# Performance work log

Hardware: AMD Instinct MI355X
Metric: run time of the kernel (lower is better)

The kernel has to match this reference:

```python
import jax, jax.numpy as jnp
import numpy as np

TEMP = 0.5   # temperature from __init__
EPS = 1e-8   # torch.nn.CosineSimilarity eps


def setup_inputs() -> dict:
    key = jax.random.key(0)
    N, D = 8192, 256
    x = jax.random.normal(key, (N, D), dtype=jnp.float32)
    # pairs: each label appears exactly twice, as required for the
    # sim[~mask].reshape(N, -1) in the original to be well-formed
    y = jnp.arange(N, dtype=jnp.int32) // 2
    return {"x": x, "y": y}


def reference(x, y):
    # cosine similarity matrix: normalize once, then one NxD @ DxN matmul
    # (equivalent to CosineSimilarity(x.unsqueeze(1), x.unsqueeze(0)) without
    #  the NxNxD intermediate)
    norm = jnp.maximum(jnp.linalg.norm(x, axis=1, keepdims=True), EPS)
    xn = x / norm
    sim = (xn @ xn.T) / TEMP                     # [N, N]

    # Original: positives = equal-label entries (row-major order, includes the
    # diagonal), logits = [positives | negatives] which is just a per-row
    # permutation of sim; labels = 0 -> CE target is the FIRST equal-label
    # column of each row. logsumexp is over the full row (all N entries).
    eq = y[:, None] == y[None, :]                # [N, N] bool
    first_pos = jnp.argmax(eq, axis=1)           # first column j with y_j == y_i
    target = jnp.take_along_axis(sim, first_pos[:, None], axis=1)[:, 0]  # [N]

    lse = jax.nn.logsumexp(sim, axis=1)          # [N]
    N = x.shape[0]
    loss = jnp.sum(lse - target) / N             # CrossEntropyLoss(sum) / N
    return loss
```

## Files before the change

### kernel.cpp

```cpp
#include <hip/hip_runtime.h>
#include <hip/hip_bf16.h>

#define D 256
#define INV_TEMP 2.0f

typedef __attribute__((ext_vector_type(8))) short short8;
typedef __attribute__((ext_vector_type(4))) float floatx4;
typedef __attribute__((ext_vector_type(4))) unsigned short ushortx4;

__device__ __forceinline__ unsigned short f2bf(float f) {
    union { float f; unsigned u; } a; a.f = f;
    unsigned r = (a.u + 0x7fffu + ((a.u >> 16) & 1u)) >> 16;
    return (unsigned short)r;
}

__device__ __forceinline__ void gload_lds16(const unsigned short* g,
                                            unsigned short* l) {
    __builtin_amdgcn_global_load_lds(
        (const __attribute__((address_space(1))) unsigned int*)g,
        (__attribute__((address_space(3))) unsigned int*)l, 16, 0, 0);
}

__global__ void nt_prep_kernel(const float* __restrict__ x,
                               unsigned short* __restrict__ xnb,
                               float* __restrict__ pair_dot,
                               float* __restrict__ rowsum,
                               float* __restrict__ gsum,
                               unsigned int* __restrict__ gcnt) {
    if (blockIdx.x == 0 && threadIdx.x == 0) { *gsum = 0.f; *gcnt = 0u; }
    if (blockIdx.x < 32) rowsum[blockIdx.x * 256 + threadIdx.x] = 0.f;
    int p    = blockIdx.x * 4 + (threadIdx.x >> 6);
    int lane = threadIdx.x & 63;
    const float4* a4 = (const float4*)(x + (size_t)(2 * p) * D);
    const float4* b4 = (const float4*)(x + (size_t)(2 * p + 1) * D);
    float4 a = a4[lane], b = b4[lane];
    float saa = a.x * a.x + a.y * a.y + a.z * a.z + a.w * a.w;
    float sbb = b.x * b.x + b.y * b.y + b.z * b.z + b.w * b.w;
    float sab = a.x * b.x + a.y * b.y + a.z * b.z + a.w * b.w;
    #pragma unroll
    for (int off = 32; off; off >>= 1) {
        saa += __shfl_xor(saa, off);
        sbb += __shfl_xor(sbb, off);
        sab += __shfl_xor(sab, off);
    }
    float inva = 1.0f / fmaxf(sqrtf(saa), 1e-8f);
    float invb = 1.0f / fmaxf(sqrtf(sbb), 1e-8f);
    ushortx4 oa, ob;
    oa.x = f2bf(a.x * inva); oa.y = f2bf(a.y * inva);
    oa.z = f2bf(a.z * inva); oa.w = f2bf(a.w * inva);
    ob.x = f2bf(b.x * invb); ob.y = f2bf(b.y * invb);
    ob.z = f2bf(b.z * invb); ob.w = f2bf(b.w * invb);
    __builtin_nontemporal_store(oa, (ushortx4*)(xnb + (size_t)(2 * p) * D) + lane);
    __builtin_nontemporal_store(ob, (ushortx4*)(xnb + (size_t)(2 * p + 1) * D) + lane);
    if (lane == 0)
        pair_dot[p] = sab * inva * invb * INV_TEMP;
}

__global__ __launch_bounds__(256, 2)
void nt_simexp_kernel(const unsigned short* __restrict__ xnb,
                      float* __restrict__ rowsum) {
    __shared__ __align__(16) unsigned short Bs[128 * 256];
    __shared__ __align__(16) unsigned short As[2][128 * 32];

    const int p  = blockIdx.x >> 4, q = blockIdx.x & 15;
    const int s1 = 63 - p;
    const int c0 = 64 - p;
    const int q0 = (p + q) & 15;

    const int tid  = threadIdx.x;
    const int wave = tid >> 6, lane = tid & 63;
    const int wm   = wave & 1, wn = wave >> 1;
    const int quad = lane >> 4, c = lane & 15;

    auto strip_of = [&](int i) { return (i < c0) ? p : s1; };
    auto bi_of    = [&](int i) { return (i < c0) ? (p + i) : (s1 + i - c0); };

    auto load_B = [&](int bj) {
        const unsigned short* src = xnb + (size_t)(bj * 128) * D;
        int rs = lane >> 5, pp = lane & 31;
        #pragma unroll
        for (int t = 0; t < 16; ++t) {
            int wl = wave * 16 + t;
            int rr = wl * 2 + rs;
            int j  = (pp & ~7) | ((pp ^ rr) & 7);
            gload_lds16(src + (size_t)rr * D + j * 8, Bs + wl * 512 + lane * 8);
        }
    };
    auto load_A = [&](int bi, int ph, unsigned short* Ab) {
        const unsigned short* src = xnb + (size_t)(bi * 128) * D + ph * 32;
        int rl = lane >> 2, pq = lane & 3;
        #pragma unroll
        for (int t = 0; t < 2; ++t) {
            int wl = wave * 2 + t;
            int rr = wl * 16 + rl;
            int j  = pq ^ ((rr >> 1) & 3);
            gload_lds16(src + (size_t)rr * D + j * 8, Ab + wl * 512 + lane * 8);
        }
    };

    floatx4 acc[4][4];
    auto compute = [&](const unsigned short* Ab, int ph) {
        const int pA = quad ^ ((c >> 1) & 3);
        const int jg = ph * 4 + quad;
        const int pB = (jg & ~7) | ((jg ^ c) & 7);
        short8 af[4], bf[4];
        #pragma unroll
        for (int mt = 0; mt < 4; ++mt)
            af[mt] = *(const short8*)(Ab + (wm * 64 + mt * 16 + c) * 32 + pA * 8);
        #pragma unroll
        for (int nt = 0; nt < 4; ++nt)
            bf[nt] = *(const short8*)(Bs + (wn * 64 + nt * 16 + c) * 256 + pB * 8);
        #pragma unroll
        for (int mt = 0; mt < 4; ++mt)
            #pragma unroll
            for (int nt = 0; nt < 4; ++nt)
                acc[mt][nt] = __builtin_amdgcn_mfma_f32_16x16x32_bf16(
                    af[mt], bf[nt], acc[mt][nt], 0, 0, 0);
    };

    int bj = strip_of(q0);
    load_B(bj);
    load_A(bi_of(q0), 0, As[0]);
    __syncthreads();

    for (int i = q0; i < 65; i += 16) {
        const int bi = bi_of(i);
        const int ni = i + 16;
        const bool have_next = (ni < 65);
        const int nbj = have_next ? strip_of(ni) : -1;
        const bool same = have_next && (nbj == bj);

        #pragma unroll
        for (int mt = 0; mt < 4; ++mt)
            #pragma unroll
            for (int nt = 0; nt < 4; ++nt)
                acc[mt][nt] = (floatx4){0.f, 0.f, 0.f, 0.f};

        #pragma unroll
        for (int ph = 0; ph < 8; ++ph) {
            if (ph < 7) load_A(bi, ph + 1, As[(ph + 1) & 1]);
            else if (same) load_A(bi_of(ni), 0, As[0]);
            compute(As[ph & 1], ph);
            __syncthreads();
        }

        if (have_next && !same) {
            load_B(nbj);
            load_A(bi_of(ni), 0, As[0]);
        }

        #pragma unroll
        for (int mt = 0; mt < 4; ++mt)
            #pragma unroll
            for (int nt = 0; nt < 4; ++nt)
                #pragma unroll
                for (int r = 0; r < 4; ++r)
                    acc[mt][nt][r] = __expf(acc[mt][nt][r] * INV_TEMP);

        #pragma unroll
        for (int mt = 0; mt < 4; ++mt) {
            float ps[4] = {0.f, 0.f, 0.f, 0.f};
            #pragma unroll
            for (int nt = 0; nt < 4; ++nt)
                #pragma unroll
                for (int r = 0; r < 4; ++r)
                    ps[r] += acc[mt][nt][r];
            #pragma unroll
            for (int off = 1; off < 16; off <<= 1)
                #pragma unroll
                for (int r = 0; r < 4; ++r)
                    ps[r] += __shfl_xor(ps[r], off);
            if (c < 4) {
                float v = (c == 0) ? ps[0] : (c == 1) ? ps[1]
                        : (c == 2) ? ps[2] : ps[3];
                atomicAdd(&rowsum[bi * 128 + wm * 64 + mt * 16 + quad * 4 + c], v);
            }
        }
        if (bi != bj) {
            #pragma unroll
            for (int nt = 0; nt < 4; ++nt) {
                float cs = 0.f;
                #pragma unroll
                for (int mt = 0; mt < 4; ++mt)
                    #pragma unroll
                    for (int r = 0; r < 4; ++r)
                        cs += acc[mt][nt][r];
                cs += __shfl_xor(cs, 16);
                cs += __shfl_xor(cs, 32);
                if (quad == 0)
                    atomicAdd(&rowsum[bj * 128 + wn * 64 + nt * 16 + c], cs);
            }
        }
        if (have_next && !same) {
            __syncthreads();
            bj = nbj;
        }
    }
}

__global__ void nt_reduce_kernel(const float* __restrict__ rowsum,
                                 const float* __restrict__ pair_dot,
                                 float* __restrict__ gsum,
                                 unsigned int* __restrict__ gcnt,
                                 float* __restrict__ out, int N) {
    __shared__ float sm[8];
    int r = blockIdx.x * 512 + threadIdx.x;
    float v = logf(rowsum[r]);
    if (r & 1) v -= pair_dot[r >> 1];
    #pragma unroll
    for (int off = 32; off; off >>= 1) v += __shfl_xor(v, off);
    int lane = threadIdx.x & 63, wv = threadIdx.x >> 6;
    if (lane == 0) sm[wv] = v;
    __syncthreads();
    if (threadIdx.x == 0) {
        float s = sm[0] + sm[1] + sm[2] + sm[3]
                + sm[4] + sm[5] + sm[6] + sm[7];
        atomicAdd(gsum, s);
        __threadfence();
        if (atomicAdd(gcnt, 1u) == 15u) {
            __threadfence();
            float t = atomicAdd(gsum, 0.0f);
            out[0] = (t - (float)N) / (float)N;
        }
    }
}

extern "C" void kernel_launch(void* const* d_in, const int* in_sizes, int n_in,
                              void* d_out, int out_size, void* d_ws, size_t ws_size,
                              hipStream_t stream) {
    const float* x = (const float*)d_in[0];
    int N = in_sizes[0] / D;

    char* ws = (char*)d_ws;
    unsigned short* xnb = (unsigned short*)ws;
    float* pair_dot  = (float*)(ws + (size_t)N * D * 2);
    float* rowsum    = pair_dot + N / 2;
    float* gsum      = rowsum + N;
    unsigned int* gcnt = (unsigned int*)(gsum + 1);

    nt_prep_kernel<<<N / 8, 256, 0, stream>>>(x, xnb, pair_dot, rowsum,
                                              gsum, gcnt);
    nt_simexp_kernel<<<512, 256, 0, stream>>>(xnb, rowsum);
    nt_reduce_kernel<<<16, 512, 0, stream>>>(rowsum, pair_dot, gsum, gcnt,
                                             (float*)d_out, N);
}
```

Measured before the change: 101.8 us.

## Use 256x256 lower-triangular tiles with 4-stage K pipeline in sim-exp kernel

Replaces the persistent strip-based 128x128 tile schedule with one block per 256x256 lower-triangular tile (528 blocks of 512 threads), mapped from the block index through a triangular-number inverse with an XCD-style remap. A and B K-slices are streamed through a 4-deep LDS ring buffer using vmcnt waits and raw barriers, and s_setprio is raised around the MFMA section. The larger tiles are meant to cut global/LDS traffic per FLOP and to remove the per-tile B reload and sync overhead. In exchange the diagonal-tile waste is larger, register pressure grows with 8x4 accumulators per wave, and the explicit vmcnt counting must match the number of outstanding loads.

```diff
diff --git a/kernel.cpp b/kernel.cpp
--- a/kernel.cpp
+++ b/kernel.cpp
@@ -56,144 +56,126 @@
         pair_dot[p] = sab * inva * invb * INV_TEMP;
 }
 
-__global__ __launch_bounds__(256, 2)
+__global__ __launch_bounds__(512, 2)
 void nt_simexp_kernel(const unsigned short* __restrict__ xnb,
                       float* __restrict__ rowsum) {
-    __shared__ __align__(16) unsigned short Bs[128 * 256];
-    __shared__ __align__(16) unsigned short As[2][128 * 32];
-
-    const int p  = blockIdx.x >> 4, q = blockIdx.x & 15;
-    const int s1 = 63 - p;
-    const int c0 = 64 - p;
-    const int q0 = (p + q) & 15;
+    __shared__ __align__(16) unsigned short As[4][256 * 32];
+    __shared__ __align__(16) unsigned short Bs[4][256 * 32];
+
+    int b = (int)blockIdx.x;
+    b = (b & 7) * 66 + (b >> 3);
+    int ti = (int)((sqrtf(8.f * (float)b + 1.f) - 1.f) * 0.5f);
+    while ((ti + 1) * (ti + 2) / 2 <= b) ++ti;
+    while (ti * (ti + 1) / 2 > b) --ti;
+    const int tj = b - ti * (ti + 1) / 2;
 
     const int tid  = threadIdx.x;
     const int wave = tid >> 6, lane = tid & 63;
-    const int wm   = wave & 1, wn = wave >> 1;
+    const int wm   = wave >> 2, wn = wave & 3;
     const int quad = lane >> 4, c = lane & 15;
-
-    auto strip_of = [&](int i) { return (i < c0) ? p : s1; };
-    auto bi_of    = [&](int i) { return (i < c0) ? (p + i) : (s1 + i - c0); };
-
-    auto load_B = [&](int bj) {
-        const unsigned short* src = xnb + (size_t)(bj * 128) * D;
-        int rs = lane >> 5, pp = lane & 31;
-        #pragma unroll
-        for (int t = 0; t < 16; ++t) {
-            int wl = wave * 16 + t;
-            int rr = wl * 2 + rs;
-            int j  = (pp & ~7) | ((pp ^ rr) & 7);
-            gload_lds16(src + (size_t)rr * D + j * 8, Bs + wl * 512 + lane * 8);
-        }
-    };
-    auto load_A = [&](int bi, int ph, unsigned short* Ab) {
-        const unsigned short* src = xnb + (size_t)(bi * 128) * D + ph * 32;
-        int rl = lane >> 2, pq = lane & 3;
+    const int pA   = quad ^ ((c >> 1) & 3);
+
+    const unsigned short* Abase = xnb + (size_t)ti * 256 * D;
+    const unsigned short* Bbase = xnb + (size_t)tj * 256 * D;
+
+    auto stage = [&](int kst, int buf) {
+        const int rl = lane >> 2, pq = lane & 3;
         #pragma unroll
         for (int t = 0; t < 2; ++t) {
             int wl = wave * 2 + t;
             int rr = wl * 16 + rl;
             int j  = pq ^ ((rr >> 1) & 3);
-            gload_lds16(src + (size_t)rr * D + j * 8, Ab + wl * 512 + lane * 8);
+            gload_lds16(Abase + (size_t)rr * D + kst * 32 + j * 8,
+                        As[buf] + wl * 512 + lane * 8);
+        }
+        #pragma unroll
+        for (int t = 0; t < 2; ++t) {
+            int wl = wave * 2 + t;
+            int rr = wl * 16 + rl;
+            int j  = pq ^ ((rr >> 1) & 3);
+            gload_lds16(Bbase + (size_t)rr * D + kst * 32 + j * 8,
+                        Bs[buf] + wl * 512 + lane * 8);
         }
     };
 
-    floatx4 acc[4][4];
-    auto compute = [&](const unsigned short* Ab, int ph) {
-        const int pA = quad ^ ((c >> 1) & 3);
-        const int jg = ph * 4 + quad;
-        const int pB = (jg & ~7) | ((jg ^ c) & 7);
-        short8 af[4], bf[4];
-        #pragma unroll
-        for (int mt = 0; mt < 4; ++mt)
-            af[mt] = *(const short8*)(Ab + (wm * 64 + mt * 16 + c) * 32 + pA * 8);
-        #pragma unroll
-        for (int nt = 0; nt < 4; ++nt)
-            bf[nt] = *(const short8*)(Bs + (wn * 64 + nt * 16 + c) * 256 + pB * 8);
-        #pragma unroll
-        for (int mt = 0; mt < 4; ++mt)
+    stage(0, 0); stage(1, 1); stage(2, 2);
+
+    floatx4 acc[8][4];
+    #pragma unroll
+    for (int mt = 0; mt < 8; ++mt)
+        #pragma unroll
+        for (int nt = 0; nt < 4; ++nt)
+            acc[mt][nt] = (floatx4){0.f, 0.f, 0.f, 0.f};
+
+    #pragma unroll
+    for (int t = 0; t < 8; ++t) {
+        asm volatile("s_waitcnt vmcnt(8)" ::: "memory");
+        __builtin_amdgcn_s_barrier();
+        asm volatile("" ::: "memory");
+
+        const int buf = t & 3;
+        short8 af[8], bf[4];
+        #pragma unroll
+        for (int mt = 0; mt < 8; ++mt)
+            af[mt] = *(const short8*)(As[buf] + (wm * 8 + mt) * 512 +
+                                      (c * 4 + pA) * 8);
+        #pragma unroll
+        for (int nt = 0; nt < 4; ++nt)
+            bf[nt] = *(const short8*)(Bs[buf] + (wn * 4 + nt) * 512 +
+                                      (c * 4 + pA) * 8);
+
+        if (t < 7) stage((t + 3) & 7, (t + 3) & 3);
+
+        __builtin_amdgcn_s_setprio(1);
+        #pragma unroll
+        for (int mt = 0; mt < 8; ++mt)
             #pragma unroll
             for (int nt = 0; nt < 4; ++nt)
                 acc[mt][nt] = __builtin_amdgcn_mfma_f32_16x16x32_bf16(
                     af[mt], bf[nt], acc[mt][nt], 0, 0, 0);
-    };
-
-    int bj = strip_of(q0);
-    load_B(bj);
-    load_A(bi_of(q0), 0, As[0]);
-    __syncthreads();
-
-    for (int i = q0; i < 65; i += 16) {
-        const int bi = bi_of(i);
-        const int ni = i + 16;
-        const bool have_next = (ni < 65);
-        const int nbj = have_next ? strip_of(ni) : -1;
-        const bool same = have_next && (nbj == bj);
-
-        #pragma unroll
-        for (int mt = 0; mt < 4; ++mt)
-            #pragma unroll
-            for (int nt = 0; nt < 4; ++nt)
-                acc[mt][nt] = (floatx4){0.f, 0.f, 0.f, 0.f};
-
-        #pragma unroll
-        for (int ph = 0; ph < 8; ++ph) {
-            if (ph < 7) load_A(bi, ph + 1, As[(ph + 1) & 1]);
-            else if (same) load_A(bi_of(ni), 0, As[0]);
-            compute(As[ph & 1], ph);
-            __syncthreads();
-        }
-
-        if (have_next && !same) {
-            load_B(nbj);
-            load_A(bi_of(ni), 0, As[0]);
-        }
-
-        #pragma unroll
-        for (int mt = 0; mt < 4; ++mt)
-            #pragma unroll
-            for (int nt = 0; nt < 4; ++nt)
+        __builtin_amdgcn_s_setprio(0);
+    }
+
+    #pragma unroll
+    for (int mt = 0; mt < 8; ++mt)
+        #pragma unroll
+        for (int nt = 0; nt < 4; ++nt)
+            #pragma unroll
+            for (int r = 0; r < 4; ++r)
+                acc[mt][nt][r] = __expf(acc[mt][nt][r] * INV_TEMP);
+
+    #pragma unroll
+    for (int mt = 0; mt < 8; ++mt) {
+        float ps[4] = {0.f, 0.f, 0.f, 0.f};
+        #pragma unroll
+        for (int nt = 0; nt < 4; ++nt)
+            #pragma unroll
+            for (int r = 0; r < 4; ++r)
+                ps[r] += acc[mt][nt][r];
+        #pragma unroll
+        for (int off = 1; off < 16; off <<= 1)
+            #pragma unroll
+            for (int r = 0; r < 4; ++r)
+                ps[r] += __shfl_xor(ps[r], off);
+        if (c < 4) {
+            float v = (c == 0) ? ps[0] : (c == 1) ? ps[1]
+                    : (c == 2) ? ps[2] : ps[3];
+            atomicAdd(&rowsum[ti * 256 + wm * 128 + mt * 16 + quad * 4 + c], v);
+        }
+    }
+    if (ti != tj) {
+        #pragma unroll
+        for (int nt = 0; nt < 4; ++nt) {
+            float cs = 0.f;
+            #pragma unroll
+            for (int mt = 0; mt < 8; ++mt)
                 #pragma unroll
                 for (int r = 0; r < 4; ++r)
-                    acc[mt][nt][r] = __expf(acc[mt][nt][r] * INV_TEMP);
-
-        #pragma unroll
-        for (int mt = 0; mt < 4; ++mt) {
-            float ps[4] = {0.f, 0.f, 0.f, 0.f};
-            #pragma unroll
-            for (int nt = 0; nt < 4; ++nt)
-                #pragma unroll
-                for (int r = 0; r < 4; ++r)
-                    ps[r] += acc[mt][nt][r];
-            #pragma unroll
-            for (int off = 1; off < 16; off <<= 1)
-                #pragma unroll
-                for (int r = 0; r < 4; ++r)
-                    ps[r] += __shfl_xor(ps[r], off);
-            if (c < 4) {
-                float v = (c == 0) ? ps[0] : (c == 1) ? ps[1]
-                        : (c == 2) ? ps[2] : ps[3];
-                atomicAdd(&rowsum[bi * 128 + wm * 64 + mt * 16 + quad * 4 + c], v);
-            }
-        }
-        if (bi != bj) {
-            #pragma unroll
-            for (int nt = 0; nt < 4; ++nt) {
-                float cs = 0.f;
-                #pragma unroll
-                for (int mt = 0; mt < 4; ++mt)
-                    #pragma unroll
-                    for (int r = 0; r < 4; ++r)
-                        cs += acc[mt][nt][r];
-                cs += __shfl_xor(cs, 16);
-                cs += __shfl_xor(cs, 32);
-                if (quad == 0)
-                    atomicAdd(&rowsum[bj * 128 + wn * 64 + nt * 16 + c], cs);
-            }
-        }
-        if (have_next && !same) {
-            __syncthreads();
-            bj = nbj;
+                    cs += acc[mt][nt][r];
+            cs += __shfl_xor(cs, 16);
+            cs += __shfl_xor(cs, 32);
+            if (quad == 0)
+                atomicAdd(&rowsum[tj * 256 + wn * 64 + nt * 16 + c], cs);
         }
     }
 }
@@ -240,7 +222,7 @@
 
     nt_prep_kernel<<<N / 8, 256, 0, stream>>>(x, xnb, pair_dot, rowsum,
                                               gsum, gcnt);
-    nt_simexp_kernel<<<512, 256, 0, stream>>>(xnb, rowsum);
+    nt_simexp_kernel<<<528, 512, 0, stream>>>(xnb, rowsum);
     nt_reduce_kernel<<<16, 512, 0, stream>>>(rowsum, pair_dot, gsum, gcnt,
                                              (float*)d_out, N);
 }
```

Measured after the change: 99.67 us, median of 4. -2.1%, faster.

## Use 256x128 tiles with 8 waves and a 4-stage A pipeline

Applied to the files above, without the earlier changes.

Restructures the symmetric sim-exp kernel so that 512-thread blocks compute 256x128 tiles over a new triangular work assignment across 256 blocks. A is staged through a 4-deep LDS ring with explicit vmcnt waits and raw barriers instead of a double buffer with __syncthreads. MFMA sections are wrapped in s_setprio to favour math issue. The intent is to reuse each B strip across twice as many rows and to hide global-to-LDS latency. The cost is more LDS per block (about 128KB) and more complex indexing, with some risk to occupancy and correctness.

```diff
diff --git a/kernel.cpp b/kernel.cpp
--- a/kernel.cpp
+++ b/kernel.cpp
@@ -56,97 +56,115 @@
         pair_dot[p] = sab * inva * invb * INV_TEMP;
 }
 
-__global__ __launch_bounds__(256, 2)
+__global__ __launch_bounds__(512, 2)
 void nt_simexp_kernel(const unsigned short* __restrict__ xnb,
                       float* __restrict__ rowsum) {
     __shared__ __align__(16) unsigned short Bs[128 * 256];
-    __shared__ __align__(16) unsigned short As[2][128 * 32];
-
-    const int p  = blockIdx.x >> 4, q = blockIdx.x & 15;
+    __shared__ __align__(16) unsigned short As[4][256 * 32];
+
+    const int p  = blockIdx.x & 31, q = blockIdx.x >> 5;
     const int s1 = 63 - p;
-    const int c0 = 64 - p;
-    const int q0 = (p + q) & 15;
-
-    const int tid  = threadIdx.x;
-    const int wave = tid >> 6, lane = tid & 63;
-    const int wm   = wave & 1, wn = wave >> 1;
+    const int cnt0 = 32 - (p >> 1);
+    const int q0 = (p + q) & 7;
+    const int ntiles = (q0 == 0) ? 5 : 4;
+
+    const int wave = threadIdx.x >> 6, lane = threadIdx.x & 63;
+    const int wm = wave & 3, wn = wave >> 2;
     const int quad = lane >> 4, c = lane & 15;
-
-    auto strip_of = [&](int i) { return (i < c0) ? p : s1; };
-    auto bi_of    = [&](int i) { return (i < c0) ? (p + i) : (s1 + i - c0); };
+    const int pA = quad ^ ((c >> 1) & 3);
+
+    auto j_of = [&](int m) { return (m < cnt0) ? p : s1; };
+    auto i_of = [&](int m) { return (m < cnt0) ? (p >> 1) + m
+                                               : (s1 >> 1) + (m - cnt0); };
 
     auto load_B = [&](int bj) {
         const unsigned short* src = xnb + (size_t)(bj * 128) * D;
         int rs = lane >> 5, pp = lane & 31;
         #pragma unroll
-        for (int t = 0; t < 16; ++t) {
-            int wl = wave * 16 + t;
+        for (int t = 0; t < 8; ++t) {
+            int wl = wave * 8 + t;
             int rr = wl * 2 + rs;
             int j  = (pp & ~7) | ((pp ^ rr) & 7);
             gload_lds16(src + (size_t)rr * D + j * 8, Bs + wl * 512 + lane * 8);
         }
     };
-    auto load_A = [&](int bi, int ph, unsigned short* Ab) {
-        const unsigned short* src = xnb + (size_t)(bi * 128) * D + ph * 32;
+    auto stage_A = [&](int i, int ph, int buf) {
+        const unsigned short* src = xnb + (size_t)(i * 256) * D + ph * 32;
         int rl = lane >> 2, pq = lane & 3;
         #pragma unroll
         for (int t = 0; t < 2; ++t) {
             int wl = wave * 2 + t;
             int rr = wl * 16 + rl;
             int j  = pq ^ ((rr >> 1) & 3);
-            gload_lds16(src + (size_t)rr * D + j * 8, Ab + wl * 512 + lane * 8);
+            gload_lds16(src + (size_t)rr * D + j * 8,
+                        As[buf] + wl * 512 + lane * 8);
         }
     };
+    auto stage_g = [&](int g) {
+        int k = g >> 3;
+        if (k >= ntiles) k = ntiles - 1;
+        stage_A(i_of(q0 + 8 * k), g & 7, g & 3);
+    };
+
+    int cur_j = j_of(q0);
+    load_B(cur_j);
+    stage_g(0); stage_g(1); stage_g(2);
 
     floatx4 acc[4][4];
-    auto compute = [&](const unsigned short* Ab, int ph) {
-        const int pA = quad ^ ((c >> 1) & 3);
-        const int jg = ph * 4 + quad;
-        const int pB = (jg & ~7) | ((jg ^ c) & 7);
-        short8 af[4], bf[4];
+    bool fullwait = true;
+
+    for (int k = 0; k < ntiles; ++k) {
+        const int m = q0 + 8 * k;
+        const int i = i_of(m), j = j_of(m);
+        if (j != cur_j) {
+            asm volatile("s_waitcnt vmcnt(0)" ::: "memory");
+            __builtin_amdgcn_s_barrier();
+            load_B(j);
+            cur_j = j;
+            fullwait = true;
+        }
+
         #pragma unroll
         for (int mt = 0; mt < 4; ++mt)
-            af[mt] = *(const short8*)(Ab + (wm * 64 + mt * 16 + c) * 32 + pA * 8);
-        #pragma unroll
-        for (int nt = 0; nt < 4; ++nt)
-            bf[nt] = *(const short8*)(Bs + (wn * 64 + nt * 16 + c) * 256 + pB * 8);
-        #pragma unroll
-        for (int mt = 0; mt < 4; ++mt)
-            #pragma unroll
-            for (int nt = 0; nt < 4; ++nt)
-                acc[mt][nt] = __builtin_amdgcn_mfma_f32_16x16x32_bf16(
-                    af[mt], bf[nt], acc[mt][nt], 0, 0, 0);
-    };
-
-    int bj = strip_of(q0);
-    load_B(bj);
-    load_A(bi_of(q0), 0, As[0]);
-    __syncthreads();
-
-    for (int i = q0; i < 65; i += 16) {
-        const int bi = bi_of(i);
-        const int ni = i + 16;
-        const bool have_next = (ni < 65);
-        const int nbj = have_next ? strip_of(ni) : -1;
-        const bool same = have_next && (nbj == bj);
-
-        #pragma unroll
-        for (int mt = 0; mt < 4; ++mt)
             #pragma unroll
             for (int nt = 0; nt < 4; ++nt)
                 acc[mt][nt] = (floatx4){0.f, 0.f, 0.f, 0.f};
 
         #pragma unroll
-        for (int ph = 0; ph < 8; ++ph) {
-            if (ph < 7) load_A(bi, ph + 1, As[(ph + 1) & 1]);
-            else if (same) load_A(bi_of(ni), 0, As[0]);
-            compute(As[ph & 1], ph);
-            __syncthreads();
-        }
-
-        if (have_next && !same) {
-            load_B(nbj);
-            load_A(bi_of(ni), 0, As[0]);
+        for (int s = 0; s < 8; ++s) {
+            const int g = k * 8 + s;
+            if (s == 0 && fullwait) {
+                asm volatile("s_waitcnt vmcnt(0)" ::: "memory");
+                fullwait = false;
+            } else {
+                asm volatile("s_waitcnt vmcnt(4)" ::: "memory");
+            }
+            __builtin_amdgcn_s_barrier();
+            asm volatile("" ::: "memory");
+
+            stage_g(g + 3);
+
+            const int buf = g & 3;
+            short8 af[4], bf[4];
+            #pragma unroll
+            for (int mt = 0; mt < 4; ++mt)
+                af[mt] = *(const short8*)(As[buf] + (wm * 4 + mt) * 512 +
+                                          c * 32 + pA * 8);
+            const int jg = s * 4 + quad;
+            const int pB = (jg & ~7) | ((jg ^ c) & 7);
+            #pragma unroll
+            for (int nt = 0; nt < 4; ++nt)
+                bf[nt] = *(const short8*)(Bs + (wn * 64 + nt * 16 + c) * 256 +
+                                          pB * 8);
+
+            __builtin_amdgcn_s_setprio(1);
+            #pragma unroll
+            for (int mt = 0; mt < 4; ++mt)
+                #pragma unroll
+                for (int nt = 0; nt < 4; ++nt)
+                    acc[mt][nt] = __builtin_amdgcn_mfma_f32_16x16x32_bf16(
+                        af[mt], bf[nt], acc[mt][nt], 0, 0, 0);
+            __builtin_amdgcn_s_setprio(0);
         }
 
         #pragma unroll
@@ -173,10 +191,10 @@
             if (c < 4) {
                 float v = (c == 0) ? ps[0] : (c == 1) ? ps[1]
                         : (c == 2) ? ps[2] : ps[3];
-                atomicAdd(&rowsum[bi * 128 + wm * 64 + mt * 16 + quad * 4 + c], v);
+                atomicAdd(&rowsum[i * 256 + wm * 64 + mt * 16 + quad * 4 + c], v);
             }
         }
-        if (bi != bj) {
+        if ((j >> 1) < i) {
             #pragma unroll
             for (int nt = 0; nt < 4; ++nt) {
                 float cs = 0.f;
@@ -188,12 +206,8 @@
                 cs += __shfl_xor(cs, 16);
                 cs += __shfl_xor(cs, 32);
                 if (quad == 0)
-                    atomicAdd(&rowsum[bj * 128 + wn * 64 + nt * 16 + c], cs);
+                    atomicAdd(&rowsum[j * 128 + wn * 64 + nt * 16 + c], cs);
             }
-        }
-        if (have_next && !same) {
-            __syncthreads();
-            bj = nbj;
         }
     }
 }
@@ -240,7 +254,7 @@
 
     nt_prep_kernel<<<N / 8, 256, 0, stream>>>(x, xnb, pair_dot, rowsum,
                                               gsum, gcnt);
-    nt_simexp_kernel<<<512, 256, 0, stream>>>(xnb, rowsum);
+    nt_simexp_kernel<<<256, 512, 0, stream>>>(xnb, rowsum);
     nt_reduce_kernel<<<16, 512, 0, stream>>>(rowsum, pair_dot, gsum, gcnt,
                                              (float*)d_out, N);
 }
```

Measured after the change: 99.63 us. 1.02x faster.

## Use 128x64 triangular tiles with 768 blocks and fuse final reduction

Applied to the files above, without the earlier changes.

Halves the B tile to 64 columns and remaps the upper-triangle tile schedule. This gives 768 blocks at an occupancy hint of 3, aiming to balance work across CUs and fill the GPU better. The separate reduce kernel is removed: the last block to finish, found with an atomic counter, computes the log-sum and target correction and writes the loss. The cost is less operand reuse per block and more atomics, plus a serial tail in the final block. There is also an odd comma-operator expression in the A-fragment load.

```diff
diff --git a/kernel.cpp b/kernel.cpp
--- a/kernel.cpp
+++ b/kernel.cpp
@@ -25,9 +25,8 @@
                                unsigned short* __restrict__ xnb,
                                float* __restrict__ pair_dot,
                                float* __restrict__ rowsum,
-                               float* __restrict__ gsum,
                                unsigned int* __restrict__ gcnt) {
-    if (blockIdx.x == 0 && threadIdx.x == 0) { *gsum = 0.f; *gcnt = 0u; }
+    if (blockIdx.x == 0 && threadIdx.x == 0) { *gcnt = 0u; }
     if (blockIdx.x < 32) rowsum[blockIdx.x * 256 + threadIdx.x] = 0.f;
     int p    = blockIdx.x * 4 + (threadIdx.x >> 6);
     int lane = threadIdx.x & 63;
@@ -56,31 +55,34 @@
         pair_dot[p] = sab * inva * invb * INV_TEMP;
 }
 
-__global__ __launch_bounds__(256, 2)
+__global__ __launch_bounds__(256, 3)
 void nt_simexp_kernel(const unsigned short* __restrict__ xnb,
-                      float* __restrict__ rowsum) {
-    __shared__ __align__(16) unsigned short Bs[128 * 256];
+                      float* __restrict__ rowsum,
+                      const float* __restrict__ pair_dot,
+                      unsigned int* __restrict__ gcnt,
+                      float* __restrict__ out, int N) {
+    __shared__ __align__(16) unsigned short Bs[64 * 256];
     __shared__ __align__(16) unsigned short As[2][128 * 32];
 
-    const int p  = blockIdx.x >> 4, q = blockIdx.x & 15;
-    const int s1 = 63 - p;
-    const int c0 = 64 - p;
-    const int q0 = (p + q) & 15;
-
-    const int tid  = threadIdx.x;
-    const int wave = tid >> 6, lane = tid & 63;
-    const int wm   = wave & 1, wn = wave >> 1;
+    const int p  = blockIdx.x & 63, q = blockIdx.x >> 6;
+    const int s1 = 127 - p;
+    const int cnt0 = 64 - (p >> 1);
+    const int q0 = (p + q) % 12;
+
+    const int wave = threadIdx.x >> 6, lane = threadIdx.x & 63;
+    const int wm = wave & 1, wn = wave >> 1;
     const int quad = lane >> 4, c = lane & 15;
 
-    auto strip_of = [&](int i) { return (i < c0) ? p : s1; };
-    auto bi_of    = [&](int i) { return (i < c0) ? (p + i) : (s1 + i - c0); };
+    auto j_of = [&](int m) { return (m < cnt0) ? p : s1; };
+    auto i_of = [&](int m) { return (m < cnt0) ? (p >> 1) + m
+                                               : (s1 >> 1) + (m - cnt0); };
 
     auto load_B = [&](int bj) {
-        const unsigned short* src = xnb + (size_t)(bj * 128) * D;
+        const unsigned short* src = xnb + (size_t)(bj * 64) * D;
         int rs = lane >> 5, pp = lane & 31;
         #pragma unroll
-        for (int t = 0; t < 16; ++t) {
-            int wl = wave * 16 + t;
+        for (int t = 0; t < 8; ++t) {
+            int wl = wave * 8 + t;
             int rr = wl * 2 + rs;
             int j  = (pp & ~7) | ((pp ^ rr) & 7);
             gload_lds16(src + (size_t)rr * D + j * 8, Bs + wl * 512 + lane * 8);
@@ -98,61 +100,61 @@
         }
     };
 
-    floatx4 acc[4][4];
+    floatx4 acc[4][2];
     auto compute = [&](const unsigned short* Ab, int ph) {
         const int pA = quad ^ ((c >> 1) & 3);
         const int jg = ph * 4 + quad;
         const int pB = (jg & ~7) | ((jg ^ c) & 7);
-        short8 af[4], bf[4];
-        #pragma unroll
-        for (int mt = 0; mt < 4; ++mt)
-            af[mt] = *(const short8*)(Ab + (wm * 64 + mt * 16 + c) * 32 + pA * 8);
-        #pragma unroll
-        for (int nt = 0; nt < 4; ++nt)
-            bf[nt] = *(const short8*)(Bs + (wn * 64 + nt * 16 + c) * 256 + pB * 8);
-        #pragma unroll
-        for (int mt = 0; mt < 4; ++mt)
-            #pragma unroll
-            for (int nt = 0; nt < 4; ++nt)
+        short8 af[4], bf[2];
+        #pragma unroll
+        for (int mt = 0; mt < 4; ++mt)
+            af[mt] = *(const short8*)(As[0] , Ab + (wm * 64 + mt * 16 + c) * 32 + pA * 8);
+        #pragma unroll
+        for (int nt = 0; nt < 2; ++nt)
+            bf[nt] = *(const short8*)(Bs + (wn * 32 + nt * 16 + c) * 256 + pB * 8);
+        #pragma unroll
+        for (int mt = 0; mt < 4; ++mt)
+            #pragma unroll
+            for (int nt = 0; nt < 2; ++nt)
                 acc[mt][nt] = __builtin_amdgcn_mfma_f32_16x16x32_bf16(
                     af[mt], bf[nt], acc[mt][nt], 0, 0, 0);
     };
 
-    int bj = strip_of(q0);
+    int bj = j_of(q0);
     load_B(bj);
-    load_A(bi_of(q0), 0, As[0]);
+    load_A(i_of(q0), 0, As[0]);
     __syncthreads();
 
-    for (int i = q0; i < 65; i += 16) {
-        const int bi = bi_of(i);
-        const int ni = i + 16;
-        const bool have_next = (ni < 65);
-        const int nbj = have_next ? strip_of(ni) : -1;
+    for (int m = q0; m < 65; m += 12) {
+        const int i = i_of(m), j = j_of(m);
+        const int nm = m + 12;
+        const bool have_next = (nm < 65);
+        const int nbj = have_next ? j_of(nm) : -1;
         const bool same = have_next && (nbj == bj);
 
         #pragma unroll
         for (int mt = 0; mt < 4; ++mt)
             #pragma unroll
-            for (int nt = 0; nt < 4; ++nt)
+            for (int nt = 0; nt < 2; ++nt)
                 acc[mt][nt] = (floatx4){0.f, 0.f, 0.f, 0.f};
 
         #pragma unroll
         for (int ph = 0; ph < 8; ++ph) {
-            if (ph < 7) load_A(bi, ph + 1, As[(ph + 1) & 1]);
-            else if (same) load_A(bi_of(ni), 0, As[0]);
+            if (ph < 7) load_A(i, ph + 1, As[(ph + 1) & 1]);
+            else if (same) load_A(i_of(nm), 0, As[0]);
             compute(As[ph & 1], ph);
             __syncthreads();
         }
 
         if (have_next && !same) {
             load_B(nbj);
-            load_A(bi_of(ni), 0, As[0]);
-        }
-
-        #pragma unroll
-        for (int mt = 0; mt < 4; ++mt)
-            #pragma unroll
-            for (int nt = 0; nt < 4; ++nt)
+            load_A(i_of(nm), 0, As[0]);
+        }
+
+        #pragma unroll
+        for (int mt = 0; mt < 4; ++mt)
+            #pragma unroll
+            for (int nt = 0; nt < 2; ++nt)
                 #pragma unroll
                 for (int r = 0; r < 4; ++r)
                     acc[mt][nt][r] = __expf(acc[mt][nt][r] * INV_TEMP);
@@ -161,7 +163,7 @@
         for (int mt = 0; mt < 4; ++mt) {
             float ps[4] = {0.f, 0.f, 0.f, 0.f};
             #pragma unroll
-            for (int nt = 0; nt < 4; ++nt)
+            for (int nt = 0; nt < 2; ++nt)
                 #pragma unroll
                 for (int r = 0; r < 4; ++r)
                     ps[r] += acc[mt][nt][r];
@@ -173,12 +175,12 @@
             if (c < 4) {
                 float v = (c == 0) ? ps[0] : (c == 1) ? ps[1]
                         : (c == 2) ? ps[2] : ps[3];
-                atomicAdd(&rowsum[bi * 128 + wm * 64 + mt * 16 + quad * 4 + c], v);
+                atomicAdd(&rowsum[i * 128 + wm * 64 + mt * 16 + quad * 4 + c], v);
             }
         }
-        if (bi != bj) {
-            #pragma unroll
-            for (int nt = 0; nt < 4; ++nt) {
+        if ((j >> 1) < i) {
+            #pragma unroll
+            for (int nt = 0; nt < 2; ++nt) {
                 float cs = 0.f;
                 #pragma unroll
                 for (int mt = 0; mt < 4; ++mt)
@@ -188,7 +190,7 @@
                 cs += __shfl_xor(cs, 16);
                 cs += __shfl_xor(cs, 32);
                 if (quad == 0)
-                    atomicAdd(&rowsum[bj * 128 + wn * 64 + nt * 16 + c], cs);
+                    atomicAdd(&rowsum[j * 64 + wn * 32 + nt * 16 + c], cs);
             }
         }
         if (have_next && !same) {
@@ -196,32 +198,32 @@
             bj = nbj;
         }
     }
-}
-
-__global__ void nt_reduce_kernel(const float* __restrict__ rowsum,
-                                 const float* __restrict__ pair_dot,
-                                 float* __restrict__ gsum,
-                                 unsigned int* __restrict__ gcnt,
-                                 float* __restrict__ out, int N) {
-    __shared__ float sm[8];
-    int r = blockIdx.x * 512 + threadIdx.x;
-    float v = logf(rowsum[r]);
-    if (r & 1) v -= pair_dot[r >> 1];
-    #pragma unroll
-    for (int off = 32; off; off >>= 1) v += __shfl_xor(v, off);
-    int lane = threadIdx.x & 63, wv = threadIdx.x >> 6;
-    if (lane == 0) sm[wv] = v;
+
+    __shared__ unsigned int lastFlag;
+    __shared__ float fsum[4];
     __syncthreads();
     if (threadIdx.x == 0) {
-        float s = sm[0] + sm[1] + sm[2] + sm[3]
-                + sm[4] + sm[5] + sm[6] + sm[7];
-        atomicAdd(gsum, s);
         __threadfence();
-        if (atomicAdd(gcnt, 1u) == 15u) {
-            __threadfence();
-            float t = atomicAdd(gsum, 0.0f);
-            out[0] = (t - (float)N) / (float)N;
-        }
+        lastFlag = (atomicAdd(gcnt, 1u) == 767u) ? 1u : 0u;
+    }
+    __syncthreads();
+    if (lastFlag) {
+        float v = 0.f;
+        #pragma unroll
+        for (int k = 0; k < 32; ++k) {
+            int r = k * 256 + threadIdx.x;
+            float rs_ = atomicAdd(&rowsum[r], 0.0f);
+            float t = logf(rs_);
+            if (r & 1) t -= pair_dot[r >> 1];
+            v += t;
+        }
+        #pragma unroll
+        for (int off = 32; off; off >>= 1) v += __shfl_xor(v, off);
+        if ((threadIdx.x & 63) == 0) fsum[threadIdx.x >> 6] = v;
+        __syncthreads();
+        if (threadIdx.x == 0)
+            out[0] = (fsum[0] + fsum[1] + fsum[2] + fsum[3] - (float)N)
+                     / (float)N;
     }
 }
 
@@ -235,12 +237,9 @@
     unsigned short* xnb = (unsigned short*)ws;
     float* pair_dot  = (float*)(ws + (size_t)N * D * 2);
     float* rowsum    = pair_dot + N / 2;
-    float* gsum      = rowsum + N;
-    unsigned int* gcnt = (unsigned int*)(gsum + 1);
-
-    nt_prep_kernel<<<N / 8, 256, 0, stream>>>(x, xnb, pair_dot, rowsum,
-                                              gsum, gcnt);
-    nt_simexp_kernel<<<512, 256, 0, stream>>>(xnb, rowsum);
-    nt_reduce_kernel<<<16, 512, 0, stream>>>(rowsum, pair_dot, gsum, gcnt,
-                                             (float*)d_out, N);
-}
+    unsigned int* gcnt = (unsigned int*)(rowsum + N);
+
+    nt_prep_kernel<<<N / 8, 256, 0, stream>>>(x, xnb, pair_dot, rowsum, gcnt);
+    nt_simexp_kernel<<<768, 256, 0, stream>>>(xnb, rowsum, pair_dot, gcnt,
+                                              (float*)d_out, N);
+}
```

Result: slower. 130.2 us (+27.9%).
